# Optimization experiments

Hardware: AMD Instinct MI355X
Metric: run time of the kernel (lower is better)

The kernel has to match this reference:

```python
import jax, jax.numpy as jnp
import numpy as np

N = 100000      # nodes_num
E = 1600000     # edges (avg degree 16)
D_IN = 256
D_OUT = 128
EPS = 1e-3      # keras BatchNormalization default epsilon
LEAKY = 0.2     # tf.nn.leaky_relu default alpha


def setup_inputs() -> dict:
    key = jax.random.key(0)
    ks = jax.random.split(key, 6)
    x = jax.random.normal(ks[0], (N, D_IN), jnp.float32)
    w = jax.random.normal(ks[1], (D_IN, D_OUT), jnp.float32) / np.float32(np.sqrt(D_IN))
    w1 = jax.random.normal(ks[2], (D_IN, D_IN), jnp.float32) / np.float32(np.sqrt(D_IN))
    w2 = jax.random.normal(ks[3], (D_IN, D_IN), jnp.float32) / np.float32(np.sqrt(D_IN))
    rows = jnp.sort(jax.random.randint(ks[4], (E,), 0, N, jnp.int32))
    cols = jax.random.randint(ks[5], (E,), 0, N, jnp.int32)
    edge_vals = jnp.ones((E,), jnp.float32)
    return {"x": x, "w": w, "w1": w1, "w2": w2,
            "edge_vals": edge_vals, "rows": rows, "cols": cols}


def reference(x, w, w1, w2, edge_vals, rows, cols):
    # Batch norm (training mode: per-feature stats over node axis, gamma=1, beta=0)
    mean = jnp.mean(x, axis=0)
    var = jnp.var(x, axis=0)
    xn = (x - mean) * jax.lax.rsqrt(var + EPS)          # [N, D_IN]

    mapped = xn @ w                                      # [N, D_OUT]
    s1 = jnp.tanh(jnp.sum((xn @ w1) * xn, axis=1))       # [N] row score
    s2 = jnp.tanh(jnp.sum((xn @ w2) * xn, axis=1))       # [N] col score

    # sparse add of adj*s1[row] and adj*s2[col], then leaky_relu on edge values
    ev = edge_vals * (s1[rows] + s2[cols])               # [E]
    ev = jnp.where(ev > 0, ev, LEAKY * ev)

    # tf.sparse.softmax: softmax over the nonzero entries of each row
    m = jax.ops.segment_max(ev, rows, num_segments=N)    # [N]
    m = jnp.where(jnp.isfinite(m), m, 0.0)               # empty rows -> 0
    ex = jnp.exp(ev - m[rows])
    denom = jax.ops.segment_sum(ex, rows, num_segments=N)
    alpha = ex / denom[rows]                             # [E] edge softmax

    # SpMM: out[i] = sum_{e: rows[e]==i} alpha[e] * mapped[cols[e]]
    out = jax.ops.segment_sum(alpha[:, None] * mapped[cols], rows, num_segments=N)
    return out  # activation is identity (activation=None)
```

## Files before the change

### kernel.cpp

```cpp
#include <hip/hip_runtime.h>

#define D_IN 256
#define D_OUT 128
#define EPS_BN 1e-3f
#define LEAKY 0.2f

typedef unsigned short u16;
typedef unsigned int u32;
typedef u16 u16x4 __attribute__((ext_vector_type(4)));
typedef u16 u16x8 __attribute__((ext_vector_type(8)));
typedef __bf16 bf16x8 __attribute__((ext_vector_type(8)));
typedef float f32x4 __attribute__((ext_vector_type(4)));

__device__ __forceinline__ float bf2f(u16 u) {
    u32 v = ((u32)u) << 16;
    return __uint_as_float(v);
}
__device__ __forceinline__ u16 f2bf(float f) {
    u32 u = __float_as_uint(f);
    u32 r = (u + 0x7FFFu + ((u >> 16) & 1u)) >> 16;
    return (u16)r;
}

__device__ __forceinline__ void bar_lgkm() {
    asm volatile("s_waitcnt lgkmcnt(0)" ::: "memory");
    __builtin_amdgcn_s_barrier();
    asm volatile("" ::: "memory");
}

__global__ void colstats_k(const float* __restrict__ x, int n,
                           float* __restrict__ sums, float* __restrict__ sqs) {
    int c = threadIdx.x;
    float s = 0.f, q = 0.f;
    for (int r = blockIdx.x; r < n; r += gridDim.x) {
        float v = x[(size_t)r * D_IN + c];
        s += v;
        q += v * v;
    }
    atomicAdd(&sums[c], s);
    atomicAdd(&sqs[c], q);
}

__global__ void finalize_k(const float* __restrict__ sums, const float* __restrict__ sqs,
                           int n, float* __restrict__ mean, float* __restrict__ inv) {
    int c = threadIdx.x;
    float m = sums[c] / (float)n;
    float v = sqs[c] / (float)n - m * m;
    mean[c] = m;
    inv[c] = rsqrtf(v + EPS_BN);
}

__global__ void prep_w_k(const float* __restrict__ w1, const float* __restrict__ w2,
                         const float* __restrict__ w, u16* __restrict__ Bth,
                         u16* __restrict__ Btl, u16* __restrict__ Wth,
                         u16* __restrict__ Wtl) {
    int idx = blockIdx.x * 256 + threadIdx.x;
    int k = idx & 255;
    int nn = idx >> 8;
    if (nn < 512) {
        float v = (nn < 256) ? w1[(size_t)k * 256 + nn]
                             : w2[(size_t)k * 256 + (nn - 256)];
        u16 h = f2bf(v);
        u16 l = f2bf(v - bf2f(h));
        Bth[(size_t)nn * 256 + k] = h;
        Btl[(size_t)nn * 256 + k] = l;
    } else {
        int nm = nn - 512;
        float v = w[(size_t)k * D_OUT + nm];
        u16 h = f2bf(v);
        u16 l = f2bf(v - bf2f(h));
        Wth[(size_t)nm * 256 + k] = h;
        Wtl[(size_t)nm * 256 + k] = l;
    }
}

__device__ __forceinline__ int kmap(int v, int g, int j) {
    return (v == 0) ? (8 * g + j) : (16 * (j >> 2) + 4 * g + (j & 3));
}

__global__ void probe_k(int* __restrict__ flagp) {
    __shared__ float Ar[16][32];
    __shared__ float Br[32][16];
    __shared__ float Dr[16][16];
    int l = threadIdx.x;
    for (int i = l; i < 512; i += 64) {
        int r = i >> 5, k = i & 31;
        Ar[r][k] = (float)(((r * 5 + k * 3) % 11) - 5);
    }
    for (int i = l; i < 512; i += 64) {
        int k = i >> 4, c = i & 15;
        Br[k][c] = (float)(((k * 3 + c * 7) % 13) - 6);
    }
    __syncthreads();
    for (int i = l; i < 256; i += 64) {
        int r = i >> 4, c = i & 15;
        float s = 0.f;
        for (int k = 0; k < 32; ++k) s += Ar[r][k] * Br[k][c];
        Dr[r][c] = s;
    }
    __syncthreads();
    int g = l >> 4, c15 = l & 15;
    int found = -1;
    for (int combo = 0; combo < 4; ++combo) {
        int va = combo >> 1, vb = combo & 1;
        u16x8 af, bfv;
#pragma unroll
        for (int j = 0; j < 8; ++j) {
            af[j] = f2bf(Ar[c15][kmap(va, g, j)]);
            bfv[j] = f2bf(Br[kmap(vb, g, j)][c15]);
        }
        f32x4 d = {0.f, 0.f, 0.f, 0.f};
        d = __builtin_amdgcn_mfma_f32_16x16x32_bf16(
            __builtin_bit_cast(bf16x8, af), __builtin_bit_cast(bf16x8, bfv), d,
            0, 0, 0);
        bool ok = true;
#pragma unroll
        for (int r = 0; r < 4; ++r) ok = ok && (d[r] == Dr[g * 4 + r][c15]);
        if (found < 0 && __all(ok)) found = combo;
    }
    if (l == 0) flagp[0] = (found < 0) ? 0 : found;
}

__device__ __forceinline__ void stage_A(const float* __restrict__ x,
                                        const float* __restrict__ mean,
                                        const float* __restrict__ inv, int m0,
                                        int n, u16* Ah, u16* Al) {
    const int tid = threadIdx.x;
    for (int i = 0; i < 16; ++i) {
        int chunk = tid + (i << 8);
        int r = chunk >> 6;
        int c4 = (chunk & 63) << 2;
        int gr = m0 + r;
        bool ok = gr < n;
        float4 v = make_float4(0.f, 0.f, 0.f, 0.f);
        if (ok) v = *(const float4*)(x + (size_t)gr * D_IN + c4);
        float4 mn = *(const float4*)(mean + c4);
        float4 iv = *(const float4*)(inv + c4);
        float a0 = ok ? (v.x - mn.x) * iv.x : 0.f;
        float a1 = ok ? (v.y - mn.y) * iv.y : 0.f;
        float a2 = ok ? (v.z - mn.z) * iv.z : 0.f;
        float a3 = ok ? (v.w - mn.w) * iv.w : 0.f;
        u16 h0 = f2bf(a0), h1 = f2bf(a1), h2 = f2bf(a2), h3 = f2bf(a3);
        u16 l0 = f2bf(a0 - bf2f(h0)), l1 = f2bf(a1 - bf2f(h1));
        u16 l2 = f2bf(a2 - bf2f(h2)), l3 = f2bf(a3 - bf2f(h3));
        int off = (r << 9) + (((c4 << 1) ^ ((r & 7) << 4)));
        u16x4 hv = {h0, h1, h2, h3};
        u16x4 lv = {l0, l1, l2, l3};
        *(u16x4*)((char*)Ah + off) = hv;
        *(u16x4*)((char*)Al + off) = lv;
    }
}

__device__ __forceinline__ void ldb_regs(const u16* __restrict__ Gh,
                                         const u16* __restrict__ Gl, int n0,
                                         int k0, int tid, u16x8 (&hv)[2],
                                         u16x8 (&lv)[2]) {
#pragma unroll
    for (int i = 0; i < 2; ++i) {
        int chunk = tid + (i << 8);
        int nl = chunk >> 3;
        int k8 = (chunk & 7) << 3;
        size_t goff = (size_t)(n0 + nl) * 256 + k0 + k8;
        hv[i] = *(const u16x8*)(Gh + goff);
        lv[i] = *(const u16x8*)(Gl + goff);
    }
}
__device__ __forceinline__ void stb_lds(u16* Bh, u16* Bl, int tid,
                                        const u16x8 (&hv)[2],
                                        const u16x8 (&lv)[2]) {
#pragma unroll
    for (int i = 0; i < 2; ++i) {
        int chunk = tid + (i << 8);
        int nl = chunk >> 3;
        int k8 = (chunk & 7) << 3;
        int off = (nl << 7) + (((k8 << 1) ^ ((nl & 7) << 4)));
        *(u16x8*)((char*)Bh + off) = hv[i];
        *(u16x8*)((char*)Bl + off) = lv[i];
    }
}

template <int V>
__device__ __forceinline__ bf16x8 ld_frag(const u16* plane, int rowByteBase,
                                          int swz, int kbyte, int g) {
    const char* p = (const char*)plane + rowByteBase;
    if constexpr (V == 0) {
        u16x8 v = *(const u16x8*)(p + ((kbyte + (g << 4)) ^ swz));
        return __builtin_bit_cast(bf16x8, v);
    } else {
        u16x4 a = *(const u16x4*)(p + ((kbyte + (g << 3)) ^ swz));
        u16x4 b = *(const u16x4*)(p + ((kbyte + 32 + (g << 3)) ^ swz));
        u16x8 v;
        v[0] = a[0]; v[1] = a[1]; v[2] = a[2]; v[3] = a[3];
        v[4] = b[0]; v[5] = b[1]; v[6] = b[2]; v[7] = b[3];
        return __builtin_bit_cast(bf16x8, v);
    }
}

template <int VA, int VB>
__device__ __forceinline__ void comp_kt(const u16* Ah, const u16* Al,
                                        const u16* Bh, const u16* Bl, int kt,
                                        int wm, int wn, int c15, int g,
                                        f32x4 (&acc)[2][2]) {
#pragma unroll
    for (int kk = 0; kk < 2; ++kk) {
        int kbA = kt * 128 + kk * 64;
        int kbB = kk * 64;
        bf16x8 ah[2], alf[2], bhf[2], blf[2];
#pragma unroll
        for (int mf = 0; mf < 2; ++mf) {
            int row = wm * 32 + mf * 16 + c15;
            int swz = (row & 7) << 4;
            ah[mf] = ld_frag<VA>(Ah, row << 9, swz, kbA, g);
            alf[mf] = ld_frag<VA>(Al, row << 9, swz, kbA, g);
        }
#pragma unroll
        for (int nf = 0; nf < 2; ++nf) {
            int nl = wn * 32 + nf * 16 + c15;
            int swz = (nl & 7) << 4;
            bhf[nf] = ld_frag<VB>(Bh, nl << 7, swz, kbB, g);
            blf[nf] = ld_frag<VB>(Bl, nl << 7, swz, kbB, g);
        }
#pragma unroll
        for (int mf = 0; mf < 2; ++mf)
#pragma unroll
            for (int nf = 0; nf < 2; ++nf) {
                acc[mf][nf] = __builtin_amdgcn_mfma_f32_16x16x32_bf16(
                    ah[mf], bhf[nf], acc[mf][nf], 0, 0, 0);
                acc[mf][nf] = __builtin_amdgcn_mfma_f32_16x16x32_bf16(
                    ah[mf], blf[nf], acc[mf][nf], 0, 0, 0);
                acc[mf][nf] = __builtin_amdgcn_mfma_f32_16x16x32_bf16(
                    alf[mf], bhf[nf], acc[mf][nf], 0, 0, 0);
            }
    }
}

template <int VA, int VB>
__device__ __forceinline__ void quadmap_body(
    const float* __restrict__ x, const u16* __restrict__ Bth,
    const u16* __restrict__ Btl, const u16* __restrict__ Wth,
    const u16* __restrict__ Wtl, const float* __restrict__ mean,
    const float* __restrict__ inv, float* __restrict__ s1,
    float* __restrict__ s2, u16* __restrict__ mapped, int n, int mapCT,
    u16* Ah, u16* Al, u16* Bh, u16* Bl) {
    const int tid = threadIdx.x;
    const int lane = tid & 63, wave = tid >> 6;
    const int g = lane >> 4, c15 = lane & 15;
    const int wm = wave >> 1, wn = wave & 1;
    const int m0 = blockIdx.x * 64;

    stage_A(x, mean, inv, m0, n, Ah, Al);
    __syncthreads();

    u16x8 rbh[2], rbl[2];
    ldb_regs(Bth, Btl, 0, 0, tid, rbh, rbl);

    float sp[2][4] = {{0.f, 0.f, 0.f, 0.f}, {0.f, 0.f, 0.f, 0.f}};

    for (int jt = 0; jt < 8; ++jt) {
        f32x4 acc[2][2];
#pragma unroll
        for (int mf = 0; mf < 2; ++mf)
#pragma unroll
            for (int nf = 0; nf < 2; ++nf) acc[mf][nf] = (f32x4){0.f, 0.f, 0.f, 0.f};

        for (int kt = 0; kt < 4; ++kt) {
            bar_lgkm();
            stb_lds(Bh, Bl, tid, rbh, rbl);
            const u16 *sH, *sL;
            int nn0, nk0;
            if (kt < 3)      { sH = Bth; sL = Btl; nn0 = jt * 64;       nk0 = (kt + 1) * 64; }
            else if (jt < 7) { sH = Bth; sL = Btl; nn0 = (jt + 1) * 64; nk0 = 0; }
            else             { sH = Wth; sL = Wtl; nn0 = 0;             nk0 = 0; }
            ldb_regs(sH, sL, nn0, nk0, tid, rbh, rbl);
            bar_lgkm();
            comp_kt<VA, VB>(Ah, Al, Bh, Bl, kt, wm, wn, c15, g, acc);
        }

        int fcol0 = (jt & 3) << 6;
#pragma unroll
        for (int mf = 0; mf < 2; ++mf) {
#pragma unroll
            for (int nf = 0; nf < 2; ++nf) {
                int col = fcol0 + wn * 32 + nf * 16 + c15;
                float mn = mean[col], ivv = inv[col];
#pragma unroll
                for (int r = 0; r < 4; ++r) {
                    int grow = m0 + wm * 32 + mf * 16 + g * 4 + r;
                    float xv = 0.f;
                    if (grow < n) xv = (x[(size_t)grow * D_IN + col] - mn) * ivv;
                    sp[mf][r] = fmaf(acc[mf][nf][r], xv, sp[mf][r]);
                }
            }
        }
        if ((jt & 3) == 3) {
            float part[2][4];
#pragma unroll
            for (int mf = 0; mf < 2; ++mf)
#pragma unroll
                for (int r = 0; r < 4; ++r) {
                    float v = sp[mf][r];
                    v += __shfl_xor(v, 1);
                    v += __shfl_xor(v, 2);
                    v += __shfl_xor(v, 4);
                    v += __shfl_xor(v, 8);
                    part[mf][r] = v;
                    sp[mf][r] = 0.f;
                }
            float* scratch = (float*)Bh;
            bar_lgkm();
            if (c15 == 0) {
#pragma unroll
                for (int mf = 0; mf < 2; ++mf)
#pragma unroll
                    for (int r = 0; r < 4; ++r) {
                        int sidx = (((((wm << 2) | g) << 1) | mf) << 3) | (r << 1) | wn;
                        scratch[sidx] = part[mf][r];
                    }
            }
            bar_lgkm();
            if (wn == 0 && c15 == 0) {
                float* dst = (jt < 4) ? s1 : s2;
#pragma unroll
                for (int mf = 0; mf < 2; ++mf)
#pragma unroll
                    for (int r = 0; r < 4; ++r) {
                        int sidx = (((((wm << 2) | g) << 1) | mf) << 3) | (r << 1);
                        float tot = scratch[sidx] + scratch[sidx | 1];
                        int grow = m0 + wm * 32 + mf * 16 + g * 4 + r;
                        if (grow < n) dst[grow] = tanhf(tot);
                    }
            }
        }
    }

    const int tiles = mapCT >> 6;
    for (int t = 0; t < tiles; ++t) {
        f32x4 acc[2][2];
#pragma unroll
        for (int mf = 0; mf < 2; ++mf)
#pragma unroll
            for (int nf = 0; nf < 2; ++nf) acc[mf][nf] = (f32x4){0.f, 0.f, 0.f, 0.f};

        for (int kt = 0; kt < 4; ++kt) {
            bar_lgkm();
            stb_lds(Bh, Bl, tid, rbh, rbl);
            int nn0 = (kt < 3) ? t * 64 : ((t + 1 < tiles) ? (t + 1) * 64 : t * 64);
            int nk0 = (kt < 3) ? (kt + 1) * 64 : 0;
            ldb_regs(Wth, Wtl, nn0, nk0, tid, rbh, rbl);
            bar_lgkm();
            comp_kt<VA, VB>(Ah, Al, Bh, Bl, kt, wm, wn, c15, g, acc);
        }
#pragma unroll
        for (int mf = 0; mf < 2; ++mf)
#pragma unroll
            for (int nf = 0; nf < 2; ++nf) {
                int si = t * 64 + wn * 32 + nf * 16 + c15;
#pragma unroll
                for (int r = 0; r < 4; ++r) {
                    int grow = m0 + wm * 32 + mf * 16 + g * 4 + r;
                    if (grow < n)
                        mapped[(size_t)grow * mapCT + si] = f2bf(acc[mf][nf][r]);
                }
            }
    }
}

__global__ __launch_bounds__(256) void quadmap_mfma_k(
    const float* __restrict__ x, const u16* __restrict__ Bth,
    const u16* __restrict__ Btl, const u16* __restrict__ Wth,
    const u16* __restrict__ Wtl, const float* __restrict__ mean,
    const float* __restrict__ inv, float* __restrict__ s1,
    float* __restrict__ s2, u16* __restrict__ mapped,
    const int* __restrict__ flagp, int n, int mapCT) {
    __shared__ u16 Ah[64 * 256];
    __shared__ u16 Al[64 * 256];
    __shared__ u16 Bh[64 * 64];
    __shared__ u16 Bl[64 * 64];
    int v = flagp[0];
    if (v == 1)
        quadmap_body<0, 1>(x, Bth, Btl, Wth, Wtl, mean, inv, s1, s2, mapped, n, mapCT, Ah, Al, Bh, Bl);
    else if (v == 2)
        quadmap_body<1, 0>(x, Bth, Btl, Wth, Wtl, mean, inv, s1, s2, mapped, n, mapCT, Ah, Al, Bh, Bl);
    else if (v == 3)
        quadmap_body<1, 1>(x, Bth, Btl, Wth, Wtl, mean, inv, s1, s2, mapped, n, mapCT, Ah, Al, Bh, Bl);
    else
        quadmap_body<0, 0>(x, Bth, Btl, Wth, Wtl, mean, inv, s1, s2, mapped, n, mapCT, Ah, Al, Bh, Bl);
}

template <int VA, int VB>
__device__ __forceinline__ void map_body(
    const float* __restrict__ x, const u16* __restrict__ Wth,
    const u16* __restrict__ Wtl, const float* __restrict__ mean,
    const float* __restrict__ inv, u16* __restrict__ mapped, int n, int c0,
    int CT, u16* Ah, u16* Al, u16* Bh, u16* Bl) {
    const int tid = threadIdx.x;
    const int lane = tid & 63, wave = tid >> 6;
    const int g = lane >> 4, c15 = lane & 15;
    const int wm = wave >> 1, wn = wave & 1;
    const int m0 = blockIdx.x * 64;

    stage_A(x, mean, inv, m0, n, Ah, Al);
    __syncthreads();

    u16x8 rbh[2], rbl[2];
    ldb_regs(Wth, Wtl, c0, 0, tid, rbh, rbl);

    const int tiles = CT >> 6;
    for (int t = 0; t < tiles; ++t) {
        f32x4 acc[2][2];
#pragma unroll
        for (int mf = 0; mf < 2; ++mf)
#pragma unroll
            for (int nf = 0; nf < 2; ++nf) acc[mf][nf] = (f32x4){0.f, 0.f, 0.f, 0.f};

        for (int kt = 0; kt < 4; ++kt) {
            bar_lgkm();
            stb_lds(Bh, Bl, tid, rbh, rbl);
            int nn0 = (kt < 3) ? c0 + t * 64
                               : c0 + ((t + 1 < tiles) ? (t + 1) * 64 : t * 64);
            int nk0 = (kt < 3) ? (kt + 1) * 64 : 0;
            ldb_regs(Wth, Wtl, nn0, nk0, tid, rbh, rbl);
            bar_lgkm();
            comp_kt<VA, VB>(Ah, Al, Bh, Bl, kt, wm, wn, c15, g, acc);
        }
#pragma unroll
        for (int mf = 0; mf < 2; ++mf)
#pragma unroll
            for (int nf = 0; nf < 2; ++nf) {
                int si = t * 64 + wn * 32 + nf * 16 + c15;
#pragma unroll
                for (int r = 0; r < 4; ++r) {
                    int grow = m0 + wm * 32 + mf * 16 + g * 4 + r;
                    if (grow < n) mapped[(size_t)grow * CT + si] = f2bf(acc[mf][nf][r]);
                }
            }
    }
}

__global__ __launch_bounds__(256) void map_mfma_k(
    const float* __restrict__ x, const u16* __restrict__ Wth,
    const u16* __restrict__ Wtl, const float* __restrict__ mean,
    const float* __restrict__ inv, u16* __restrict__ mapped, int n, int c0,
    int CT, const int* __restrict__ flagp) {
    __shared__ u16 Ah[64 * 256];
    __shared__ u16 Al[64 * 256];
    __shared__ u16 Bh[64 * 64];
    __shared__ u16 Bl[64 * 64];
    int v = flagp[0];
    if (v == 1) map_body<0, 1>(x, Wth, Wtl, mean, inv, mapped, n, c0, CT, Ah, Al, Bh, Bl);
    else if (v == 2) map_body<1, 0>(x, Wth, Wtl, mean, inv, mapped, n, c0, CT, Ah, Al, Bh, Bl);
    else if (v == 3) map_body<1, 1>(x, Wth, Wtl, mean, inv, mapped, n, c0, CT, Ah, Al, Bh, Bl);
    else map_body<0, 0>(x, Wth, Wtl, mean, inv, mapped, n, c0, CT, Ah, Al, Bh, Bl);
}

template <typename OT>
__global__ __launch_bounds__(256) void gemm_map_k(const float* __restrict__ x,
                                                  const float* __restrict__ w,
                                                  const float* __restrict__ mean,
                                                  const float* __restrict__ inv,
                                                  OT* __restrict__ outp, int n,
                                                  int c0, int CT) {
    __shared__ float As[64][68];
    __shared__ float Bs[64][68];
    const int tid = threadIdx.x;
    const int tx = tid & 15, ty = tid >> 4;
    const int m0 = blockIdx.x * 64;
    const int tiles = (CT + 63) >> 6;

    for (int t = 0; t < tiles; ++t) {
        const int jt = c0 + (t << 6);
        float acc[4][4];
#pragma unroll
        for (int a = 0; a < 4; ++a)
#pragma unroll
            for (int b = 0; b < 4; ++b) acc[a][b] = 0.f;

        for (int kt = 0; kt < D_IN; kt += 64) {
#pragma unroll
            for (int i = 0; i < 4; ++i) {
                int f4 = tid + 256 * i;
                int r = f4 >> 4;
                int c4 = (f4 & 15) << 2;
                float4 o;
                int gr = m0 + r;
                if (gr < n) {
                    float4 v = *(const float4*)(x + (size_t)gr * D_IN + kt + c4);
                    float4 mn = *(const float4*)(mean + kt + c4);
                    float4 iv = *(const float4*)(inv + kt + c4);
                    o.x = (v.x - mn.x) * iv.x;
                    o.y = (v.y - mn.y) * iv.y;
                    o.z = (v.z - mn.z) * iv.z;
                    o.w = (v.w - mn.w) * iv.w;
                } else {
                    o = make_float4(0.f, 0.f, 0.f, 0.f);
                }
                *(float4*)&As[r][c4] = o;
            }
#pragma unroll
            for (int i = 0; i < 4; ++i) {
                int f4 = tid + 256 * i;
                int r = f4 >> 4;
                int c4 = (f4 & 15) << 2;
                int jc = jt + c4;
                float4 bv = (jc < D_OUT)
                                ? *(const float4*)(w + (size_t)(kt + r) * D_OUT + jc)
                                : make_float4(0.f, 0.f, 0.f, 0.f);
                *(float4*)&Bs[r][c4] = bv;
            }
            __syncthreads();
#pragma unroll 8
            for (int k = 0; k < 64; ++k) {
                float4 bv = *(const float4*)&Bs[k][tx << 2];
                float a0 = As[(ty << 2) + 0][k];
                float a1 = As[(ty << 2) + 1][k];
                float a2 = As[(ty << 2) + 2][k];
                float a3 = As[(ty << 2) + 3][k];
                acc[0][0] = fmaf(a0, bv.x, acc[0][0]);
                acc[0][1] = fmaf(a0, bv.y, acc[0][1]);
                acc[0][2] = fmaf(a0, bv.z, acc[0][2]);
                acc[0][3] = fmaf(a0, bv.w, acc[0][3]);
                acc[1][0] = fmaf(a1, bv.x, acc[1][0]);
                acc[1][1] = fmaf(a1, bv.y, acc[1][1]);
                acc[1][2] = fmaf(a1, bv.z, acc[1][2]);
                acc[1][3] = fmaf(a1, bv.w, acc[1][3]);
                acc[2][0] = fmaf(a2, bv.x, acc[2][0]);
                acc[2][1] = fmaf(a2, bv.y, acc[2][1]);
                acc[2][2] = fmaf(a2, bv.z, acc[2][2]);
                acc[2][3] = fmaf(a2, bv.w, acc[2][3]);
                acc[3][0] = fmaf(a3, bv.x, acc[3][0]);
                acc[3][1] = fmaf(a3, bv.y, acc[3][1]);
                acc[3][2] = fmaf(a3, bv.z, acc[3][2]);
                acc[3][3] = fmaf(a3, bv.w, acc[3][3]);
            }
            __syncthreads();
        }
        int si = (jt - c0) + (tx << 2);
        if (si < CT) {
#pragma unroll
            for (int a = 0; a < 4; ++a) {
                int gm = m0 + (ty << 2) + a;
                if (gm < n) {
                    ushort4 pk;
                    pk.x = f2bf(acc[a][0]);
                    pk.y = f2bf(acc[a][1]);
                    pk.z = f2bf(acc[a][2]);
                    pk.w = f2bf(acc[a][3]);
                    *(ushort4*)((u16*)outp + (size_t)gm * CT + si) = pk;
                }
            }
        }
    }
}

__global__ void build_rowptr_k(const int* __restrict__ rows, int E, int n,
                               int* __restrict__ rp) {
    int e = blockIdx.x * blockDim.x + threadIdx.x;
    if (e >= E) return;
    int r = rows[e];
    int prev = (e == 0) ? -1 : rows[e - 1];
    for (int q = prev + 1; q <= r; ++q) rp[q] = e;
    if (e == E - 1) {
        for (int q = r + 1; q <= n; ++q) rp[q] = E;
    }
}

template <bool WRITE_ALPHA>
__global__ __launch_bounds__(256) void row_softmax_k(
    const int* __restrict__ row_ptr, const int* __restrict__ cols,
    const float* __restrict__ ev, const float* __restrict__ s1,
    const float* __restrict__ s2, float* __restrict__ rmax,
    float* __restrict__ rsm, float* __restrict__ alpha, int n) {
    int wave = threadIdx.x >> 6;
    int lane = threadIdx.x & 63;
    int row = blockIdx.x * 4 + wave;
    if (row >= n) return;
    int e0 = row_ptr[row], e1 = row_ptr[row + 1];
    if (e0 >= e1) {
        if (lane == 0) {
            rmax[row] = 0.f;
            rsm[row] = 0.f;
        }
        return;
    }
    float s1r = s1[row];
    float mx = -1e30f;
    for (int e = e0 + lane; e < e1; e += 64) {
        float v = ev[e] * (s1r + s2[cols[e]]);
        v = v > 0.f ? v : LEAKY * v;
        mx = fmaxf(mx, v);
    }
#pragma unroll
    for (int off = 32; off; off >>= 1) mx = fmaxf(mx, __shfl_xor(mx, off));
    float sm = 0.f;
    for (int e = e0 + lane; e < e1; e += 64) {
        float v = ev[e] * (s1r + s2[cols[e]]);
        v = v > 0.f ? v : LEAKY * v;
        sm += __expf(v - mx);
    }
#pragma unroll
    for (int off = 32; off; off >>= 1) sm += __shfl_xor(sm, off);
    float rsm_v = 1.f / sm;
    if (lane == 0) {
        rmax[row] = mx;
        rsm[row] = rsm_v;
    }
    if constexpr (WRITE_ALPHA) {
        for (int e = e0 + lane; e < e1; e += 64) {
            float v = ev[e] * (s1r + s2[cols[e]]);
            v = v > 0.f ? v : LEAKY * v;
            alpha[e] = __expf(v - mx) * rsm_v;
        }
    }
}

template <bool HAS_ALPHA>
__global__ __launch_bounds__(256) void attn_gather2_k(
    const int* __restrict__ row_ptr, const int* __restrict__ cols,
    const float* __restrict__ alpha, const float* __restrict__ ev,
    const float* __restrict__ s1, const float* __restrict__ s2,
    const float* __restrict__ rmax, const float* __restrict__ rsm,
    const u16* __restrict__ mapped, float* __restrict__ outp, int n, int c0,
    int CT) {
    const int wave = threadIdx.x >> 6;
    const int lane = threadIdx.x & 63;
    const int row = blockIdx.x * 4 + wave;
    if (row >= n) return;
    const int e0 = row_ptr[row], e1 = row_ptr[row + 1];
    float* orow = outp + (size_t)row * D_OUT + c0;
    const int nu = CT >> 1;
    const bool act = lane < nu;
    if (e0 >= e1) {
        if (act) *(float2*)(orow + (lane << 1)) = make_float2(0.f, 0.f);
        return;
    }
    float s1r = 0.f, mxv = 0.f, rsv = 0.f;
    if constexpr (!HAS_ALPHA) {
        s1r = s1[row];
        mxv = rmax[row];
        rsv = rsm[row];
    }
    const u32* map32 = (const u32*)mapped;
    float ox = 0.f, oy = 0.f;
    int e = e0;
    while (e < e1) {
        int cnt = min(e1 - e, 64);
        int ce = 0;
        float ae = 0.f;
        if (lane < cnt) {
            int ee = e + lane;
            ce = cols[ee];
            if constexpr (HAS_ALPHA) {
                ae = alpha[ee];
            } else {
                float v = ev[ee] * (s1r + s2[ce]);
                v = v > 0.f ? v : LEAKY * v;
                ae = __expf(v - mxv) * rsv;
            }
        }
        for (int j0 = 0; j0 < cnt; j0 += 8) {
            int cv[8];
            float av[8];
            u32 mv[8];
#pragma unroll
            for (int j = 0; j < 8; ++j) {
                cv[j] = __shfl(ce, j0 + j);
                av[j] = __shfl(ae, j0 + j);
            }
#pragma unroll
            for (int j = 0; j < 8; ++j)
                mv[j] = act ? map32[(size_t)cv[j] * nu + lane] : 0u;
#pragma unroll
            for (int j = 0; j < 8; ++j) {
                ox = fmaf(av[j], bf2f((u16)(mv[j] & 0xffffu)), ox);
                oy = fmaf(av[j], bf2f((u16)(mv[j] >> 16)), oy);
            }
        }
        e += cnt;
    }
    if (act) *(float2*)(orow + (lane << 1)) = make_float2(ox, oy);
}

extern "C" void kernel_launch(void* const* d_in, const int* in_sizes, int n_in,
                              void* d_out, int out_size, void* d_ws, size_t ws_size,
                              hipStream_t stream) {
    const float* x  = (const float*)d_in[0];
    const float* w  = (const float*)d_in[1];
    const float* w1 = (const float*)d_in[2];
    const float* w2 = (const float*)d_in[3];
    const float* ev = (const float*)d_in[4];
    const int* rows = (const int*)d_in[5];
    const int* cols = (const int*)d_in[6];
    float* out = (float*)d_out;

    const int N = in_sizes[0] / D_IN;
    const int E = in_sizes[4];

    char* base = (char*)d_ws;
    size_t off = 0;
    auto alloc = [&](size_t bytes) -> char* {
        off = (off + 255) & ~(size_t)255;
        char* p = base + off;
        off += bytes;
        return p;
    };
    float* sums  = (float*)alloc(256 * 4);
    float* sqs   = (float*)alloc(256 * 4);
    float* mean  = (float*)alloc(256 * 4);
    float* inv   = (float*)alloc(256 * 4);
    float* s1    = (float*)alloc((size_t)N * 4);
    float* s2    = (float*)alloc((size_t)N * 4);
    float* rmax  = (float*)alloc((size_t)N * 4);
    float* rsm   = (float*)alloc((size_t)N * 4);
    int* row_ptr = (int*)alloc((size_t)(N + 1) * 4);
    int* flag    = (int*)alloc(256);
    u16* Bth = (u16*)alloc((size_t)512 * 256 * 2);
    u16* Btl = (u16*)alloc((size_t)512 * 256 * 2);
    u16* Wth = (u16*)alloc((size_t)128 * 256 * 2);
    u16* Wtl = (u16*)alloc((size_t)128 * 256 * 2);
    size_t head0 = off;

    size_t alpha_bytes = (size_t)E * 4;
    auto fits_alpha = [&](size_t mapped_bytes) {
        size_t o = (head0 + 255) & ~(size_t)255;
        o += alpha_bytes;
        o = (o + 255) & ~(size_t)255;
        return o + mapped_bytes <= ws_size;
    };
    auto fits_noalpha = [&](size_t mapped_bytes) {
        size_t o = (head0 + 255) & ~(size_t)255;
        return o + mapped_bytes <= ws_size;
    };

    bool has_alpha;
    int CT;
    if (fits_alpha((size_t)N * 128 * 2)) {
        has_alpha = true; CT = 128;
    } else if (fits_alpha((size_t)N * 64 * 2)) {
        has_alpha = true; CT = 64;
    } else if (fits_noalpha((size_t)N * 32 * 2)) {
        has_alpha = false; CT = 32;
    } else if (fits_noalpha((size_t)N * 16 * 2)) {
        has_alpha = false; CT = 16;
    } else {
        has_alpha = false; CT = 8;
    }
    float* alpha = has_alpha ? (float*)alloc(alpha_bytes) : nullptr;
    u16* mapped = (u16*)alloc((size_t)N * CT * 2);

    hipMemsetAsync(sums, 0, 512 * sizeof(float), stream);
    colstats_k<<<512, 256, 0, stream>>>(x, N, sums, sqs);
    finalize_k<<<1, 256, 0, stream>>>(sums, sqs, N, mean, inv);
    prep_w_k<<<640, 256, 0, stream>>>(w1, w2, w, Bth, Btl, Wth, Wtl);
    probe_k<<<1, 64, 0, stream>>>(flag);

    int qb = (N + 63) / 64;
    int mapCT = (CT >= 64) ? CT : 0;
    quadmap_mfma_k<<<qb, 256, 0, stream>>>(x, Bth, Btl, Wth, Wtl, mean, inv, s1,
                                           s2, mapped, flag, N, mapCT);

    build_rowptr_k<<<(E + 255) / 256, 256, 0, stream>>>(rows, E, N, row_ptr);
    int ab = (N + 3) / 4;
    if (has_alpha) {
        row_softmax_k<true><<<ab, 256, 0, stream>>>(row_ptr, cols, ev, s1, s2,
                                                    rmax, rsm, alpha, N);
    } else {
        row_softmax_k<false><<<ab, 256, 0, stream>>>(row_ptr, cols, ev, s1, s2,
                                                     rmax, rsm, nullptr, N);
    }

    if (CT == 128) {
        attn_gather2_k<true><<<ab, 256, 0, stream>>>(
            row_ptr, cols, alpha, ev, s1, s2, rmax, rsm, mapped, out, N, 0, CT);
    } else if (CT == 64) {
        attn_gather2_k<true><<<ab, 256, 0, stream>>>(
            row_ptr, cols, alpha, ev, s1, s2, rmax, rsm, mapped, out, N, 0, 64);
        map_mfma_k<<<qb, 256, 0, stream>>>(x, Wth, Wtl, mean, inv, mapped, N, 64,
                                           64, flag);
        attn_gather2_k<true><<<ab, 256, 0, stream>>>(
            row_ptr, cols, alpha, ev, s1, s2, rmax, rsm, mapped, out, N, 64, 64);
    } else {
        for (int c0 = 0; c0 < D_OUT; c0 += CT) {
            gemm_map_k<u16><<<qb, 256, 0, stream>>>(x, w, mean, inv, mapped, N,
                                                    c0, CT);
            attn_gather2_k<false><<<ab, 256, 0, stream>>>(
                row_ptr, cols, nullptr, ev, s1, s2, rmax, rsm, mapped, out, N,
                c0, CT);
        }
    }
}
```

Measured before the change: 584.7 us.

## Fuse edge softmax into gather, double-buffer B tiles, vectorize column stats

Removes the separate row_softmax kernel and the alpha buffer. The gather kernel now computes each row's max and sum with wave shuffles, using a fast path for rows of degree up to 64 and a three-pass path for larger rows. The quadratic-form MFMA kernel now double-buffers half-size B tiles in LDS so global loads overlap compute, with one barrier per step. The column-stats kernel uses float4 loads and launches fewer blocks. Together these cut a kernel launch and the alpha write and read, and reduce synchronization, at the cost of recomputing edge scores in the gather.

```diff
diff --git a/kernel.cpp b/kernel.cpp
--- a/kernel.cpp
+++ b/kernel.cpp
@@ -30,15 +30,25 @@
 
 __global__ void colstats_k(const float* __restrict__ x, int n,
                            float* __restrict__ sums, float* __restrict__ sqs) {
-    int c = threadIdx.x;
-    float s = 0.f, q = 0.f;
-    for (int r = blockIdx.x; r < n; r += gridDim.x) {
-        float v = x[(size_t)r * D_IN + c];
-        s += v;
-        q += v * v;
-    }
-    atomicAdd(&sums[c], s);
-    atomicAdd(&sqs[c], q);
+    int c4 = (threadIdx.x & 63) << 2;
+    int rp = threadIdx.x >> 6;
+    float s0 = 0.f, s1 = 0.f, s2 = 0.f, s3 = 0.f;
+    float q0 = 0.f, q1 = 0.f, q2 = 0.f, q3 = 0.f;
+    for (int r = blockIdx.x * 4 + rp; r < n; r += gridDim.x * 4) {
+        float4 v = *(const float4*)(x + (size_t)r * D_IN + c4);
+        s0 += v.x; q0 += v.x * v.x;
+        s1 += v.y; q1 += v.y * v.y;
+        s2 += v.z; q2 += v.z * v.z;
+        s3 += v.w; q3 += v.w * v.w;
+    }
+    atomicAdd(&sums[c4 + 0], s0);
+    atomicAdd(&sums[c4 + 1], s1);
+    atomicAdd(&sums[c4 + 2], s2);
+    atomicAdd(&sums[c4 + 3], s3);
+    atomicAdd(&sqs[c4 + 0], q0);
+    atomicAdd(&sqs[c4 + 1], q1);
+    atomicAdd(&sqs[c4 + 2], q2);
+    atomicAdd(&sqs[c4 + 3], q3);
 }
 
 __global__ void finalize_k(const float* __restrict__ sums, const float* __restrict__ sqs,
@@ -151,34 +161,6 @@
     }
 }
 
-__device__ __forceinline__ void ldb_regs(const u16* __restrict__ Gh,
-                                         const u16* __restrict__ Gl, int n0,
-                                         int k0, int tid, u16x8 (&hv)[2],
-                                         u16x8 (&lv)[2]) {
-#pragma unroll
-    for (int i = 0; i < 2; ++i) {
-        int chunk = tid + (i << 8);
-        int nl = chunk >> 3;
-        int k8 = (chunk & 7) << 3;
-        size_t goff = (size_t)(n0 + nl) * 256 + k0 + k8;
-        hv[i] = *(const u16x8*)(Gh + goff);
-        lv[i] = *(const u16x8*)(Gl + goff);
-    }
-}
-__device__ __forceinline__ void stb_lds(u16* Bh, u16* Bl, int tid,
-                                        const u16x8 (&hv)[2],
-                                        const u16x8 (&lv)[2]) {
-#pragma unroll
-    for (int i = 0; i < 2; ++i) {
-        int chunk = tid + (i << 8);
-        int nl = chunk >> 3;
-        int k8 = (chunk & 7) << 3;
-        int off = (nl << 7) + (((k8 << 1) ^ ((nl & 7) << 4)));
-        *(u16x8*)((char*)Bh + off) = hv[i];
-        *(u16x8*)((char*)Bl + off) = lv[i];
-    }
-}
-
 template <int V>
 __device__ __forceinline__ bf16x8 ld_frag(const u16* plane, int rowByteBase,
                                           int swz, int kbyte, int g) {
@@ -196,42 +178,107 @@
     }
 }
 
+__device__ __forceinline__ void ldb_half(const u16* __restrict__ Gh,
+                                         const u16* __restrict__ Gl, int n0,
+                                         int k0, int tid, u16x8& hv, u16x8& lv) {
+    int nl = tid >> 2;
+    int k8 = (tid & 3) << 3;
+    size_t goff = (size_t)(n0 + nl) * 256 + k0 + k8;
+    hv = *(const u16x8*)(Gh + goff);
+    lv = *(const u16x8*)(Gl + goff);
+}
+__device__ __forceinline__ void stb_half(u16* Bh, u16* Bl, int tid,
+                                         const u16x8& hv, const u16x8& lv) {
+    int nl = tid >> 2;
+    int kb = (tid & 3) << 4;
+    int off = (nl << 6) + (kb ^ (((nl >> 1) & 3) << 4));
+    *(u16x8*)((char*)Bh + off) = hv;
+    *(u16x8*)((char*)Bl + off) = lv;
+}
+template <int V>
+__device__ __forceinline__ bf16x8 ld_bfrag(const u16* Bp, int nl, int g) {
+    const char* p = (const char*)Bp + (nl << 6);
+    int swz = ((nl >> 1) & 3) << 4;
+    if constexpr (V == 0) {
+        u16x8 v = *(const u16x8*)(p + ((g << 4) ^ swz));
+        return __builtin_bit_cast(bf16x8, v);
+    } else {
+        u16x4 a = *(const u16x4*)(p + ((g << 3) ^ swz));
+        u16x4 b = *(const u16x4*)(p + ((32 + (g << 3)) ^ swz));
+        u16x8 v;
+        v[0] = a[0]; v[1] = a[1]; v[2] = a[2]; v[3] = a[3];
+        v[4] = b[0]; v[5] = b[1]; v[6] = b[2]; v[7] = b[3];
+        return __builtin_bit_cast(bf16x8, v);
+    }
+}
+
 template <int VA, int VB>
-__device__ __forceinline__ void comp_kt(const u16* Ah, const u16* Al,
-                                        const u16* Bh, const u16* Bl, int kt,
-                                        int wm, int wn, int c15, int g,
-                                        f32x4 (&acc)[2][2]) {
-#pragma unroll
-    for (int kk = 0; kk < 2; ++kk) {
-        int kbA = kt * 128 + kk * 64;
-        int kbB = kk * 64;
-        bf16x8 ah[2], alf[2], bhf[2], blf[2];
-#pragma unroll
-        for (int mf = 0; mf < 2; ++mf) {
-            int row = wm * 32 + mf * 16 + c15;
-            int swz = (row & 7) << 4;
-            ah[mf] = ld_frag<VA>(Ah, row << 9, swz, kbA, g);
-            alf[mf] = ld_frag<VA>(Al, row << 9, swz, kbA, g);
-        }
+__device__ __forceinline__ void comp_half(const u16* Ah, const u16* Al,
+                                          const u16* Bh, const u16* Bl, int kbA,
+                                          int wm, int wn, int c15, int g,
+                                          f32x4 (&acc)[2][2]) {
+    bf16x8 ah[2], alf[2], bhf[2], blf[2];
+#pragma unroll
+    for (int mf = 0; mf < 2; ++mf) {
+        int row = wm * 32 + mf * 16 + c15;
+        int swz = (row & 7) << 4;
+        ah[mf] = ld_frag<VA>(Ah, row << 9, swz, kbA, g);
+        alf[mf] = ld_frag<VA>(Al, row << 9, swz, kbA, g);
+    }
+#pragma unroll
+    for (int nf = 0; nf < 2; ++nf) {
+        int nl = wn * 32 + nf * 16 + c15;
+        bhf[nf] = ld_bfrag<VB>(Bh, nl, g);
+        blf[nf] = ld_bfrag<VB>(Bl, nl, g);
+    }
+#pragma unroll
+    for (int mf = 0; mf < 2; ++mf)
 #pragma unroll
         for (int nf = 0; nf < 2; ++nf) {
-            int nl = wn * 32 + nf * 16 + c15;
-            int swz = (nl & 7) << 4;
-            bhf[nf] = ld_frag<VB>(Bh, nl << 7, swz, kbB, g);
-            blf[nf] = ld_frag<VB>(Bl, nl << 7, swz, kbB, g);
-        }
-#pragma unroll
-        for (int mf = 0; mf < 2; ++mf)
-#pragma unroll
-            for (int nf = 0; nf < 2; ++nf) {
-                acc[mf][nf] = __builtin_amdgcn_mfma_f32_16x16x32_bf16(
-                    ah[mf], bhf[nf], acc[mf][nf], 0, 0, 0);
-                acc[mf][nf] = __builtin_amdgcn_mfma_f32_16x16x32_bf16(
-                    ah[mf], blf[nf], acc[mf][nf], 0, 0, 0);
-                acc[mf][nf] = __builtin_amdgcn_mfma_f32_16x16x32_bf16(
-                    alf[mf], bhf[nf], acc[mf][nf], 0, 0, 0);
-            }
-    }
+            acc[mf][nf] = __builtin_amdgcn_mfma_f32_16x16x32_bf16(
+                ah[mf], bhf[nf], acc[mf][nf], 0, 0, 0);
+            acc[mf][nf] = __builtin_amdgcn_mfma_f32_16x16x32_bf16(
+                ah[mf], blf[nf], acc[mf][nf], 0, 0, 0);
+            acc[mf][nf] = __builtin_amdgcn_mfma_f32_16x16x32_bf16(
+                alf[mf], bhf[nf], acc[mf][nf], 0, 0, 0);
+        }
+}
+
+__device__ __forceinline__ void nxt_src(int u, int mapCT,
+                                        const u16* __restrict__ Bth,
+                                        const u16* __restrict__ Btl,
+                                        const u16* __restrict__ Wth,
+                                        const u16* __restrict__ Wtl,
+                                        const u16*& Gh, const u16*& Gl, int& n0,
+                                        int& k0) {
+    if (u < 64) {
+        Gh = Bth; Gl = Btl;
+        n0 = (u >> 3) << 6;
+        k0 = (u & 7) << 5;
+    } else {
+        int um = u - 64;
+        int t = um >> 3;
+        int tmax = (mapCT >= 64) ? ((mapCT >> 6) - 1) : 0;
+        if (t > tmax) t = tmax;
+        Gh = Wth; Gl = Wtl;
+        n0 = t << 6;
+        k0 = (um & 7) << 5;
+    }
+}
+
+template <int VA, int VB>
+__device__ __forceinline__ void pipe_step(const u16* Ah, const u16* Al,
+                                          const u16* Bch, const u16* Bcl,
+                                          u16* Bwh, u16* Bwl, u16x8& h, u16x8& l,
+                                          const u16* __restrict__ Gh,
+                                          const u16* __restrict__ Gl, int n0,
+                                          int k0, int kbA, int tid, int wm,
+                                          int wn, int c15, int g,
+                                          f32x4 (&acc)[2][2]) {
+    stb_half(Bwh, Bwl, tid, h, l);
+    ldb_half(Gh, Gl, n0, k0, tid, h, l);
+    comp_half<VA, VB>(Ah, Al, Bch, Bcl, kbA, wm, wn, c15, g, acc);
+    bar_lgkm();
 }
 
 template <int VA, int VB>
@@ -241,7 +288,7 @@
     const u16* __restrict__ Wtl, const float* __restrict__ mean,
     const float* __restrict__ inv, float* __restrict__ s1,
     float* __restrict__ s2, u16* __restrict__ mapped, int n, int mapCT,
-    u16* Ah, u16* Al, u16* Bh, u16* Bl) {
+    u16* Ah, u16* Al, u16* Bh0, u16* Bl0, u16* Bh1, u16* Bl1) {
     const int tid = threadIdx.x;
     const int lane = tid & 63, wave = tid >> 6;
     const int g = lane >> 4, c15 = lane & 15;
@@ -251,29 +298,39 @@
     stage_A(x, mean, inv, m0, n, Ah, Al);
     __syncthreads();
 
-    u16x8 rbh[2], rbl[2];
-    ldb_regs(Bth, Btl, 0, 0, tid, rbh, rbl);
+    u16x8 hA, lA, hB, lB;
+    {
+        const u16 *Gh, *Gl; int n0, k0;
+        nxt_src(0, mapCT, Bth, Btl, Wth, Wtl, Gh, Gl, n0, k0);
+        ldb_half(Gh, Gl, n0, k0, tid, hA, lA);
+        nxt_src(1, mapCT, Bth, Btl, Wth, Wtl, Gh, Gl, n0, k0);
+        ldb_half(Gh, Gl, n0, k0, tid, hB, lB);
+        stb_half(Bh0, Bl0, tid, hA, lA);
+        nxt_src(2, mapCT, Bth, Btl, Wth, Wtl, Gh, Gl, n0, k0);
+        ldb_half(Gh, Gl, n0, k0, tid, hA, lA);
+        bar_lgkm();
+    }
 
     float sp[2][4] = {{0.f, 0.f, 0.f, 0.f}, {0.f, 0.f, 0.f, 0.f}};
+    float* red = (float*)Bh1;
 
     for (int jt = 0; jt < 8; ++jt) {
+        const int u0 = jt * 8;
         f32x4 acc[2][2];
 #pragma unroll
         for (int mf = 0; mf < 2; ++mf)
 #pragma unroll
             for (int nf = 0; nf < 2; ++nf) acc[mf][nf] = (f32x4){0.f, 0.f, 0.f, 0.f};
 
-        for (int kt = 0; kt < 4; ++kt) {
-            bar_lgkm();
-            stb_lds(Bh, Bl, tid, rbh, rbl);
-            const u16 *sH, *sL;
-            int nn0, nk0;
-            if (kt < 3)      { sH = Bth; sL = Btl; nn0 = jt * 64;       nk0 = (kt + 1) * 64; }
-            else if (jt < 7) { sH = Bth; sL = Btl; nn0 = (jt + 1) * 64; nk0 = 0; }
-            else             { sH = Wth; sL = Wtl; nn0 = 0;             nk0 = 0; }
-            ldb_regs(sH, sL, nn0, nk0, tid, rbh, rbl);
-            bar_lgkm();
-            comp_kt<VA, VB>(Ah, Al, Bh, Bl, kt, wm, wn, c15, g, acc);
+#pragma unroll
+        for (int sp2 = 0; sp2 < 4; ++sp2) {
+            const u16 *Gh, *Gl; int n0, k0;
+            nxt_src(u0 + sp2 * 2 + 3, mapCT, Bth, Btl, Wth, Wtl, Gh, Gl, n0, k0);
+            pipe_step<VA, VB>(Ah, Al, Bh0, Bl0, Bh1, Bl1, hB, lB, Gh, Gl, n0, k0,
+                              (sp2 * 2) * 64, tid, wm, wn, c15, g, acc);
+            nxt_src(u0 + sp2 * 2 + 4, mapCT, Bth, Btl, Wth, Wtl, Gh, Gl, n0, k0);
+            pipe_step<VA, VB>(Ah, Al, Bh1, Bl1, Bh0, Bl0, hA, lA, Gh, Gl, n0, k0,
+                              (sp2 * 2 + 1) * 64, tid, wm, wn, c15, g, acc);
         }
 
         int fcol0 = (jt & 3) << 6;
@@ -306,15 +363,13 @@
                     part[mf][r] = v;
                     sp[mf][r] = 0.f;
                 }
-            float* scratch = (float*)Bh;
-            bar_lgkm();
             if (c15 == 0) {
 #pragma unroll
                 for (int mf = 0; mf < 2; ++mf)
 #pragma unroll
                     for (int r = 0; r < 4; ++r) {
                         int sidx = (((((wm << 2) | g) << 1) | mf) << 3) | (r << 1) | wn;
-                        scratch[sidx] = part[mf][r];
+                        red[sidx] = part[mf][r];
                     }
             }
             bar_lgkm();
@@ -325,30 +380,33 @@
 #pragma unroll
                     for (int r = 0; r < 4; ++r) {
                         int sidx = (((((wm << 2) | g) << 1) | mf) << 3) | (r << 1);
-                        float tot = scratch[sidx] + scratch[sidx | 1];
+                        float tot = red[sidx] + red[sidx | 1];
                         int grow = m0 + wm * 32 + mf * 16 + g * 4 + r;
                         if (grow < n) dst[grow] = tanhf(tot);
                     }
             }
+            bar_lgkm();
         }
     }
 
     const int tiles = mapCT >> 6;
     for (int t = 0; t < tiles; ++t) {
+        const int u0 = 64 + t * 8;
         f32x4 acc[2][2];
 #pragma unroll
         for (int mf = 0; mf < 2; ++mf)
 #pragma unroll
             for (int nf = 0; nf < 2; ++nf) acc[mf][nf] = (f32x4){0.f, 0.f, 0.f, 0.f};
 
-        for (int kt = 0; kt < 4; ++kt) {
-            bar_lgkm();
-            stb_lds(Bh, Bl, tid, rbh, rbl);
-            int nn0 = (kt < 3) ? t * 64 : ((t + 1 < tiles) ? (t + 1) * 64 : t * 64);
-            int nk0 = (kt < 3) ? (kt + 1) * 64 : 0;
-            ldb_regs(Wth, Wtl, nn0, nk0, tid, rbh, rbl);
-            bar_lgkm();
-            comp_kt<VA, VB>(Ah, Al, Bh, Bl, kt, wm, wn, c15, g, acc);
+#pragma unroll
+        for (int sp2 = 0; sp2 < 4; ++sp2) {
+            const u16 *Gh, *Gl; int n0, k0;
+            nxt_src(u0 + sp2 * 2 + 3, mapCT, Bth, Btl, Wth, Wtl, Gh, Gl, n0, k0);
+            pipe_step<VA, VB>(Ah, Al, Bh0, Bl0, Bh1, Bl1, hB, lB, Gh, Gl, n0, k0,
+                              (sp2 * 2) * 64, tid, wm, wn, c15, g, acc);
+            nxt_src(u0 + sp2 * 2 + 4, mapCT, Bth, Btl, Wth, Wtl, Gh, Gl, n0, k0);
+            pipe_step<VA, VB>(Ah, Al, Bh1, Bl1, Bh0, Bl0, hA, lA, Gh, Gl, n0, k0,
+                              (sp2 * 2 + 1) * 64, tid, wm, wn, c15, g, acc);
         }
 #pragma unroll
         for (int mf = 0; mf < 2; ++mf)
@@ -374,17 +432,84 @@
     const int* __restrict__ flagp, int n, int mapCT) {
     __shared__ u16 Ah[64 * 256];
     __shared__ u16 Al[64 * 256];
-    __shared__ u16 Bh[64 * 64];
-    __shared__ u16 Bl[64 * 64];
+    __shared__ u16 Bh0[64 * 32];
+    __shared__ u16 Bl0[64 * 32];
+    __shared__ u16 Bh1[64 * 32];
+    __shared__ u16 Bl1[64 * 32];
     int v = flagp[0];
     if (v == 1)
-        quadmap_body<0, 1>(x, Bth, Btl, Wth, Wtl, mean, inv, s1, s2, mapped, n, mapCT, Ah, Al, Bh, Bl);
+        quadmap_body<0, 1>(x, Bth, Btl, Wth, Wtl, mean, inv, s1, s2, mapped, n, mapCT, Ah, Al, Bh0, Bl0, Bh1, Bl1);
     else if (v == 2)
-        quadmap_body<1, 0>(x, Bth, Btl, Wth, Wtl, mean, inv, s1, s2, mapped, n, mapCT, Ah, Al, Bh, Bl);
+        quadmap_body<1, 0>(x, Bth, Btl, Wth, Wtl, mean, inv, s1, s2, mapped, n, mapCT, Ah, Al, Bh0, Bl0, Bh1, Bl1);
     else if (v == 3)
-        quadmap_body<1, 1>(x, Bth, Btl, Wth, Wtl, mean, inv, s1, s2, mapped, n, mapCT, Ah, Al, Bh, Bl);
+        quadmap_body<1, 1>(x, Bth, Btl, Wth, Wtl, mean, inv, s1, s2, mapped, n, mapCT, Ah, Al, Bh0, Bl0, Bh1, Bl1);
     else
-        quadmap_body<0, 0>(x, Bth, Btl, Wth, Wtl, mean, inv, s1, s2, mapped, n, mapCT, Ah, Al, Bh, Bl);
+        quadmap_body<0, 0>(x, Bth, Btl, Wth, Wtl, mean, inv, s1, s2, mapped, n, mapCT, Ah, Al, Bh0, Bl0, Bh1, Bl1);
+}
+
+__device__ __forceinline__ void ldb_regs(const u16* __restrict__ Gh,
+                                         const u16* __restrict__ Gl, int n0,
+                                         int k0, int tid, u16x8 (&hv)[2],
+                                         u16x8 (&lv)[2]) {
+#pragma unroll
+    for (int i = 0; i < 2; ++i) {
+        int chunk = tid + (i << 8);
+        int nl = chunk >> 3;
+        int k8 = (chunk & 7) << 3;
+        size_t goff = (size_t)(n0 + nl) * 256 + k0 + k8;
+        hv[i] = *(const u16x8*)(Gh + goff);
+        lv[i] = *(const u16x8*)(Gl + goff);
+    }
+}
+__device__ __forceinline__ void stb_lds(u16* Bh, u16* Bl, int tid,
+                                        const u16x8 (&hv)[2],
+                                        const u16x8 (&lv)[2]) {
+#pragma unroll
+    for (int i = 0; i < 2; ++i) {
+        int chunk = tid + (i << 8);
+        int nl = chunk >> 3;
+        int k8 = (chunk & 7) << 3;
+        int off = (nl << 7) + (((k8 << 1) ^ ((nl & 7) << 4)));
+        *(u16x8*)((char*)Bh + off) = hv[i];
+        *(u16x8*)((char*)Bl + off) = lv[i];
+    }
+}
+template <int VA, int VB>
+__device__ __forceinline__ void comp_kt(const u16* Ah, const u16* Al,
+                                        const u16* Bh, const u16* Bl, int kt,
+                                        int wm, int wn, int c15, int g,
+                                        f32x4 (&acc)[2][2]) {
+#pragma unroll
+    for (int kk = 0; kk < 2; ++kk) {
+        int kbA = kt * 128 + kk * 64;
+        int kbB = kk * 64;
+        bf16x8 ah[2], alf[2], bhf[2], blf[2];
+#pragma unroll
+        for (int mf = 0; mf < 2; ++mf) {
+            int row = wm * 32 + mf * 16 + c15;
+            int swz = (row & 7) << 4;
+            ah[mf] = ld_frag<VA>(Ah, row << 9, swz, kbA, g);
+            alf[mf] = ld_frag<VA>(Al, row << 9, swz, kbA, g);
+        }
+#pragma unroll
+        for (int nf = 0; nf < 2; ++nf) {
+            int nl = wn * 32 + nf * 16 + c15;
+            int swz = (nl & 7) << 4;
+            bhf[nf] = ld_frag<VB>(Bh, nl << 7, swz, kbB, g);
+            blf[nf] = ld_frag<VB>(Bl, nl << 7, swz, kbB, g);
+        }
+#pragma unroll
+        for (int mf = 0; mf < 2; ++mf)
+#pragma unroll
+            for (int nf = 0; nf < 2; ++nf) {
+                acc[mf][nf] = __builtin_amdgcn_mfma_f32_16x16x32_bf16(
+                    ah[mf], bhf[nf], acc[mf][nf], 0, 0, 0);
+                acc[mf][nf] = __builtin_amdgcn_mfma_f32_16x16x32_bf16(
+                    ah[mf], blf[nf], acc[mf][nf], 0, 0, 0);
+                acc[mf][nf] = __builtin_amdgcn_mfma_f32_16x16x32_bf16(
+                    alf[mf], bhf[nf], acc[mf][nf], 0, 0, 0);
+            }
+    }
 }
 
 template <int VA, int VB>
@@ -564,63 +689,11 @@
     }
 }
 
-template <bool WRITE_ALPHA>
-__global__ __launch_bounds__(256) void row_softmax_k(
+__global__ __launch_bounds__(256) void attn_fused_k(
     const int* __restrict__ row_ptr, const int* __restrict__ cols,
     const float* __restrict__ ev, const float* __restrict__ s1,
-    const float* __restrict__ s2, float* __restrict__ rmax,
-    float* __restrict__ rsm, float* __restrict__ alpha, int n) {
-    int wave = threadIdx.x >> 6;
-    int lane = threadIdx.x & 63;
-    int row = blockIdx.x * 4 + wave;
-    if (row >= n) return;
-    int e0 = row_ptr[row], e1 = row_ptr[row + 1];
-    if (e0 >= e1) {
-        if (lane == 0) {
-            rmax[row] = 0.f;
-            rsm[row] = 0.f;
-        }
-        return;
-    }
-    float s1r = s1[row];
-    float mx = -1e30f;
-    for (int e = e0 + lane; e < e1; e += 64) {
-        float v = ev[e] * (s1r + s2[cols[e]]);
-        v = v > 0.f ? v : LEAKY * v;
-        mx = fmaxf(mx, v);
-    }
-#pragma unroll
-    for (int off = 32; off; off >>= 1) mx = fmaxf(mx, __shfl_xor(mx, off));
-    float sm = 0.f;
-    for (int e = e0 + lane; e < e1; e += 64) {
-        float v = ev[e] * (s1r + s2[cols[e]]);
-        v = v > 0.f ? v : LEAKY * v;
-        sm += __expf(v - mx);
-    }
-#pragma unroll
-    for (int off = 32; off; off >>= 1) sm += __shfl_xor(sm, off);
-    float rsm_v = 1.f / sm;
-    if (lane == 0) {
-        rmax[row] = mx;
-        rsm[row] = rsm_v;
-    }
-    if constexpr (WRITE_ALPHA) {
-        for (int e = e0 + lane; e < e1; e += 64) {
-            float v = ev[e] * (s1r + s2[cols[e]]);
-            v = v > 0.f ? v : LEAKY * v;
-            alpha[e] = __expf(v - mx) * rsm_v;
-        }
-    }
-}
-
-template <bool HAS_ALPHA>
-__global__ __launch_bounds__(256) void attn_gather2_k(
-    const int* __restrict__ row_ptr, const int* __restrict__ cols,
-    const float* __restrict__ alpha, const float* __restrict__ ev,
-    const float* __restrict__ s1, const float* __restrict__ s2,
-    const float* __restrict__ rmax, const float* __restrict__ rsm,
-    const u16* __restrict__ mapped, float* __restrict__ outp, int n, int c0,
-    int CT) {
+    const float* __restrict__ s2, const u16* __restrict__ mapped,
+    float* __restrict__ outp, int n, int c0, int CT) {
     const int wave = threadIdx.x >> 6;
     const int lane = threadIdx.x & 63;
     const int row = blockIdx.x * 4 + wave;
@@ -633,38 +706,36 @@
         if (act) *(float2*)(orow + (lane << 1)) = make_float2(0.f, 0.f);
         return;
     }
-    float s1r = 0.f, mxv = 0.f, rsv = 0.f;
-    if constexpr (!HAS_ALPHA) {
-        s1r = s1[row];
-        mxv = rmax[row];
-        rsv = rsm[row];
-    }
+    const float s1r = s1[row];
+    const int deg = e1 - e0;
     const u32* map32 = (const u32*)mapped;
     float ox = 0.f, oy = 0.f;
-    int e = e0;
-    while (e < e1) {
-        int cnt = min(e1 - e, 64);
-        int ce = 0;
-        float ae = 0.f;
-        if (lane < cnt) {
-            int ee = e + lane;
-            ce = cols[ee];
-            if constexpr (HAS_ALPHA) {
-                ae = alpha[ee];
-            } else {
-                float v = ev[ee] * (s1r + s2[ce]);
-                v = v > 0.f ? v : LEAKY * v;
-                ae = __expf(v - mxv) * rsv;
-            }
-        }
-        for (int j0 = 0; j0 < cnt; j0 += 8) {
+
+    if (deg <= 64) {
+        int myc = 0;
+        float myv = 0.f;
+        if (lane < deg) {
+            int ee = e0 + lane;
+            myc = cols[ee];
+            float v = ev[ee] * (s1r + s2[myc]);
+            myv = v > 0.f ? v : LEAKY * v;
+        }
+        float mx = (lane < deg) ? myv : -1e30f;
+#pragma unroll
+        for (int off = 32; off; off >>= 1) mx = fmaxf(mx, __shfl_xor(mx, off));
+        float sm = (lane < deg) ? __expf(myv - mx) : 0.f;
+#pragma unroll
+        for (int off = 32; off; off >>= 1) sm += __shfl_xor(sm, off);
+        float rsv = 1.f / sm;
+        float amine = (lane < deg) ? __expf(myv - mx) * rsv : 0.f;
+        for (int j0 = 0; j0 < deg; j0 += 8) {
             int cv[8];
             float av[8];
             u32 mv[8];
 #pragma unroll
             for (int j = 0; j < 8; ++j) {
-                cv[j] = __shfl(ce, j0 + j);
-                av[j] = __shfl(ae, j0 + j);
+                cv[j] = __shfl(myc, j0 + j);
+                av[j] = __shfl(amine, j0 + j);
             }
 #pragma unroll
             for (int j = 0; j < 8; ++j)
@@ -675,7 +746,56 @@
                 oy = fmaf(av[j], bf2f((u16)(mv[j] >> 16)), oy);
             }
         }
-        e += cnt;
+    } else {
+        float mx = -1e30f;
+        for (int e = e0 + lane; e < e1; e += 64) {
+            float v = ev[e] * (s1r + s2[cols[e]]);
+            v = v > 0.f ? v : LEAKY * v;
+            mx = fmaxf(mx, v);
+        }
+#pragma unroll
+        for (int off = 32; off; off >>= 1) mx = fmaxf(mx, __shfl_xor(mx, off));
+        float sm = 0.f;
+        for (int e = e0 + lane; e < e1; e += 64) {
+            float v = ev[e] * (s1r + s2[cols[e]]);
+            v = v > 0.f ? v : LEAKY * v;
+            sm += __expf(v - mx);
+        }
+#pragma unroll
+        for (int off = 32; off; off >>= 1) sm += __shfl_xor(sm, off);
+        float rsv = 1.f / sm;
+        int e = e0;
+        while (e < e1) {
+            int cnt = min(e1 - e, 64);
+            int ce = 0;
+            float ae = 0.f;
+            if (lane < cnt) {
+                int ee = e + lane;
+                ce = cols[ee];
+                float v = ev[ee] * (s1r + s2[ce]);
+                v = v > 0.f ? v : LEAKY * v;
+                ae = __expf(v - mx) * rsv;
+            }
+            for (int j0 = 0; j0 < cnt; j0 += 8) {
+                int cv[8];
+                float av[8];
+                u32 mv[8];
+#pragma unroll
+                for (int j = 0; j < 8; ++j) {
+                    cv[j] = __shfl(ce, j0 + j);
+                    av[j] = __shfl(ae, j0 + j);
+                }
+#pragma unroll
+                for (int j = 0; j < 8; ++j)
+                    mv[j] = act ? map32[(size_t)cv[j] * nu + lane] : 0u;
+#pragma unroll
+                for (int j = 0; j < 8; ++j) {
+                    ox = fmaf(av[j], bf2f((u16)(mv[j] & 0xffffu)), ox);
+                    oy = fmaf(av[j], bf2f((u16)(mv[j] >> 16)), oy);
+                }
+            }
+            e += cnt;
+        }
     }
     if (act) *(float2*)(orow + (lane << 1)) = make_float2(ox, oy);
 }
@@ -709,8 +829,6 @@
     float* inv   = (float*)alloc(256 * 4);
     float* s1    = (float*)alloc((size_t)N * 4);
     float* s2    = (float*)alloc((size_t)N * 4);
-    float* rmax  = (float*)alloc((size_t)N * 4);
-    float* rsm   = (float*)alloc((size_t)N * 4);
     int* row_ptr = (int*)alloc((size_t)(N + 1) * 4);
     int* flag    = (int*)alloc(256);
     u16* Bth = (u16*)alloc((size_t)512 * 256 * 2);
@@ -719,36 +837,21 @@
     u16* Wtl = (u16*)alloc((size_t)128 * 256 * 2);
     size_t head0 = off;
 
-    size_t alpha_bytes = (size_t)E * 4;
-    auto fits_alpha = [&](size_t mapped_bytes) {
-        size_t o = (head0 + 255) & ~(size_t)255;
-        o += alpha_bytes;
-        o = (o + 255) & ~(size_t)255;
-        return o + mapped_bytes <= ws_size;
-    };
-    auto fits_noalpha = [&](size_t mapped_bytes) {
+    auto fits = [&](size_t mapped_bytes) {
         size_t o = (head0 + 255) & ~(size_t)255;
         return o + mapped_bytes <= ws_size;
     };
 
-    bool has_alpha;
     int CT;
-    if (fits_alpha((size_t)N * 128 * 2)) {
-        has_alpha = true; CT = 128;
-    } else if (fits_alpha((size_t)N * 64 * 2)) {
-        has_alpha = true; CT = 64;
-    } else if (fits_noalpha((size_t)N * 32 * 2)) {
-        has_alpha = false; CT = 32;
-    } else if (fits_noalpha((size_t)N * 16 * 2)) {
-        has_alpha = false; CT = 16;
-    } else {
-        has_alpha = false; CT = 8;
-    }
-    float* alpha = has_alpha ? (float*)alloc(alpha_bytes) : nullptr;
+    if (fits((size_t)N * 128 * 2)) CT = 128;
+    else if (fits((size_t)N * 64 * 2)) CT = 64;
+    else if (fits((size_t)N * 32 * 2)) CT = 32;
+    else if (fits((size_t)N * 16 * 2)) CT = 16;
+    else CT = 8;
     u16* mapped = (u16*)alloc((size_t)N * CT * 2);
 
     hipMemsetAsync(sums, 0, 512 * sizeof(float), stream);
-    colstats_k<<<512, 256, 0, stream>>>(x, N, sums, sqs);
+    colstats_k<<<256, 256, 0, stream>>>(x, N, sums, sqs);
     finalize_k<<<1, 256, 0, stream>>>(sums, sqs, N, mean, inv);
     prep_w_k<<<640, 256, 0, stream>>>(w1, w2, w, Bth, Btl, Wth, Wtl);
     probe_k<<<1, 64, 0, stream>>>(flag);
@@ -760,31 +863,23 @@
 
     build_rowptr_k<<<(E + 255) / 256, 256, 0, stream>>>(rows, E, N, row_ptr);
     int ab = (N + 3) / 4;
-    if (has_alpha) {
-        row_softmax_k<true><<<ab, 256, 0, stream>>>(row_ptr, cols, ev, s1, s2,
-                                                    rmax, rsm, alpha, N);
-    } else {
-        row_softmax_k<false><<<ab, 256, 0, stream>>>(row_ptr, cols, ev, s1, s2,
-                                                     rmax, rsm, nullptr, N);
-    }
 
     if (CT == 128) {
-        attn_gather2_k<true><<<ab, 256, 0, stream>>>(
-            row_ptr, cols, alpha, ev, s1, s2, rmax, rsm, mapped, out, N, 0, CT);
+        attn_fused_k<<<ab, 256, 0, stream>>>(row_ptr, cols, ev, s1, s2, mapped,
+                                             out, N, 0, CT);
     } else if (CT == 64) {
-        attn_gather2_k<true><<<ab, 256, 0, stream>>>(
-            row_ptr, cols, alpha, ev, s1, s2, rmax, rsm, mapped, out, N, 0, 64);
+        attn_fused_k<<<ab, 256, 0, stream>>>(row_ptr, cols, ev, s1, s2, mapped,
+                                             out, N, 0, 64);
         map_mfma_k<<<qb, 256, 0, stream>>>(x, Wth, Wtl, mean, inv, mapped, N, 64,
                                            64, flag);
-        attn_gather2_k<true><<<ab, 256, 0, stream>>>(
-            row_ptr, cols, alpha, ev, s1, s2, rmax, rsm, mapped, out, N, 64, 64);
+        attn_fused_k<<<ab, 256, 0, stream>>>(row_ptr, cols, ev, s1, s2, mapped,
+                                             out, N, 64, 64);
     } else {
         for (int c0 = 0; c0 < D_OUT; c0 += CT) {
             gemm_map_k<u16><<<qb, 256, 0, stream>>>(x, w, mean, inv, mapped, N,
                                                     c0, CT);
-            attn_gather2_k<false><<<ab, 256, 0, stream>>>(
-                row_ptr, cols, nullptr, ev, s1, s2, rmax, rsm, mapped, out, N,
-                c0, CT);
-        }
-    }
-}
+            attn_fused_k<<<ab, 256, 0, stream>>>(row_ptr, cols, ev, s1, s2,
+                                                 mapped, out, N, c0, CT);
+        }
+    }
+}
```

Result: slower. 612.9 us (+4.8%).
